# Performance work log

Measured on AMD Instinct MI355X. Metric: run time of the kernel, lower is better.

## Reference

```python
import jax, jax.numpy as jnp
import numpy as np

N = 50000
E = 800000
D = 256
EPS_FA = 0.1      # FAConv eps (x_0 skip weight)
EPS_LN = 1e-5     # LayerNorm eps


def setup_inputs() -> dict:
    key = jax.random.key(0)
    ks = jax.random.split(key, 8)
    node = jax.random.normal(ks[0], (N, D), dtype=jnp.float32)
    node_0 = jax.random.normal(ks[1], (N, D), dtype=jnp.float32)
    edge_index = jax.random.randint(ks[2], (2, E), 0, N, dtype=jnp.int64)
    edge_attr = jax.random.uniform(ks[3], (E,), dtype=jnp.float32)
    batch_ptr = jnp.sort(jax.random.randint(ks[4], (9,), 0, N, dtype=jnp.int64))
    # FAConv attention vectors: Linear(channels, 1, bias=False) -> [D]
    att_l = jax.random.normal(ks[5], (D,), dtype=jnp.float32) / np.sqrt(D)
    att_r = jax.random.normal(ks[6], (D,), dtype=jnp.float32) / np.sqrt(D)
    ln_weight = jnp.ones((D,), dtype=jnp.float32)
    ln_bias = jnp.zeros((D,), dtype=jnp.float32)
    return {"node": node, "node_0": node_0, "edge_index": edge_index,
            "edge_attr": edge_attr, "batch_ptr": batch_ptr,
            "att_l": att_l, "att_r": att_r,
            "ln_weight": ln_weight, "ln_bias": ln_bias}


def reference(node, node_0, edge_index, edge_attr, batch_ptr, att_l, att_r, ln_weight, ln_bias):
    src = edge_index[0]  # j (source)
    dst = edge_index[1]  # i (target)
    # per-node attention scalars
    a_l = node @ att_l   # [N]
    a_r = node @ att_r   # [N]
    # per-edge coefficient: tanh(alpha_j + alpha_i) * edge_weight
    coef = jnp.tanh(a_l[src] + a_r[dst]) * edge_attr          # [E]
    msg = node[src] * coef[:, None]                           # [E, D]
    agg = jax.ops.segment_sum(msg, dst, num_segments=N)       # [N, D]
    out = agg + EPS_FA * node_0
    # LayerNorm (mode='node'): per-node over features; batch_ptr unused in node mode
    mean = out.mean(axis=-1, keepdims=True)
    var = out.var(axis=-1, keepdims=True)
    out = (out - mean) * jax.lax.rsqrt(var + EPS_LN) * ln_weight + ln_bias
    return jax.nn.relu(out)
```

## Files before the change

### kernel.cpp

```cpp
#include <hip/hip_runtime.h>
#include <math.h>

#define NN 50000
#define NE 800000
#define D 256
#define EPS_FA 0.1f
#define EPS_LN 1e-5f
#define MAXDEG 48
#define ALPHA_BLOCKS (NN / 4)
#define EDGE_BLOCKS ((NE + 255) / 256)
#define EB8 ((NE + 2047) / 2048)

typedef unsigned int u32x2 __attribute__((ext_vector_type(2)));
typedef float        f32x4 __attribute__((ext_vector_type(4)));


__device__ __forceinline__ unsigned bf16_bits(float f) {
    unsigned u = __float_as_uint(f);
    u += 0x7FFFu + ((u >> 16) & 1u);
    return u >> 16;
}
__device__ __forceinline__ float bf16_lo(unsigned u) { return __uint_as_float(u << 16); }
__device__ __forceinline__ float bf16_hi(unsigned u) { return __uint_as_float(u & 0xFFFF0000u); }

__device__ __forceinline__ float fast_tanh(float x) {
    x = fminf(fmaxf(x, -15.0f), 15.0f);
    float e2 = __expf(2.0f * x);
    return 1.0f - 2.0f * __fdividef(1.0f, e2 + 1.0f);
}

template<int DS>
__global__ __launch_bounds__(256) void alpha_fill_t(
    const float* __restrict__ node,
    const float* __restrict__ att_l,
    const float* __restrict__ att_r,
    const int*   __restrict__ edge_index,
    const float* __restrict__ edge_attr,
    float* __restrict__ a_l,
    float* __restrict__ a_r,
    uint2* __restrict__ node_bf,
    int*      __restrict__ deg,
    unsigned* __restrict__ slots)
{
    int b = blockIdx.x;
    if (b < EB8) {
        int base = b * 2048 + threadIdx.x;
        int src[8], dst[8];
        unsigned attr[8];
        #pragma unroll
        for (int i = 0; i < 8; i++) {
            int e = base + i * 256;
            bool ok = e < NE;
            src[i]  = ok ? __builtin_nontemporal_load(&edge_index[e]) : 0;
            dst[i]  = ok ? __builtin_nontemporal_load(&edge_index[NE + e]) : -1;
            attr[i] = ok ? bf16_bits(__builtin_nontemporal_load(&edge_attr[e])) : 0u;
        }
        int rank[8];
        #pragma unroll
        for (int i = 0; i < 8; i++)
            rank[i] = (dst[i] >= 0) ? atomicAdd(&deg[dst[i] * DS], 1) : MAXDEG;
        #pragma unroll
        for (int i = 0; i < 8; i++)
            if (dst[i] >= 0 && rank[i] < MAXDEG)
                slots[dst[i] * MAXDEG + rank[i]] = (unsigned)src[i] | (attr[i] << 16);
    } else {
        int wid  = ((b - EB8) * 256 + threadIdx.x) >> 6;
        int lane = threadIdx.x & 63;
        f32x4 v = __builtin_nontemporal_load((const f32x4*)(node + (size_t)wid * D) + lane);
        float4 l = ((const float4*)att_l)[lane];
        float4 r = ((const float4*)att_r)[lane];
        uint2 p;
        p.x = bf16_bits(v.x) | (bf16_bits(v.y) << 16);
        p.y = bf16_bits(v.z) | (bf16_bits(v.w) << 16);
        node_bf[(size_t)wid * 64 + lane] = p;
        float sl = v.x * l.x + v.y * l.y + v.z * l.z + v.w * l.w;
        float sr = v.x * r.x + v.y * r.y + v.z * r.z + v.w * r.w;
        #pragma unroll
        for (int off = 32; off > 0; off >>= 1) {
            sl += __shfl_down(sl, off, 64);
            sr += __shfl_down(sr, off, 64);
        }
        if (lane == 0) { a_l[wid] = sl; a_r[wid] = sr; }
    }
}

template<int DS>
__global__ __launch_bounds__(256) void gather_ln_bf16_t(
    const uint2* __restrict__ node_bf,
    const float* __restrict__ node_0,
    const float* __restrict__ a_l,
    const float* __restrict__ a_r,
    const int*      __restrict__ deg,
    const unsigned* __restrict__ slots,
    const float* __restrict__ w,
    const float* __restrict__ b,
    float* __restrict__ out)
{
    int n    = (blockIdx.x * 256 + threadIdx.x) >> 6;
    int lane = threadIdx.x & 63;

    f32x4 z = __builtin_nontemporal_load((const f32x4*)(node_0 + (size_t)n * D) + lane);
    float4 acc;
    acc.x = EPS_FA * z.x; acc.y = EPS_FA * z.y;
    acc.z = EPS_FA * z.z; acc.w = EPS_FA * z.w;

    int d = min(__builtin_nontemporal_load(&deg[n * DS]), MAXDEG);
    const unsigned* sl = slots + n * MAXDEG;

    unsigned myslot = (lane < d) ? __builtin_nontemporal_load(&sl[lane]) : 0u;
    int      myrow  = (int)(myslot & 0xFFFF);
    float    ar     = a_r[n];
    float    mycoef = 0.0f;
    if (lane < d)
        mycoef = fast_tanh(a_l[myrow] + ar) * bf16_hi(myslot);

    int k = 0;
    for (; k + 15 < d; k += 16) {
        int row[16]; float c[16]; uint2 r[16];
        #pragma unroll
        for (int i = 0; i < 16; i++) {
            row[i] = __shfl(myrow,  k + i, 64);
            c[i]   = __shfl(mycoef, k + i, 64);
        }
        #pragma unroll
        for (int i = 0; i < 16; i++)
            r[i] = node_bf[(size_t)row[i] * 64 + lane];
        #pragma unroll
        for (int i = 0; i < 16; i++) {
            acc.x += c[i] * bf16_lo(r[i].x); acc.y += c[i] * bf16_hi(r[i].x);
            acc.z += c[i] * bf16_lo(r[i].y); acc.w += c[i] * bf16_hi(r[i].y);
        }
    }
    for (; k + 7 < d; k += 8) {
        int row[8]; float c[8]; uint2 r[8];
        #pragma unroll
        for (int i = 0; i < 8; i++) {
            row[i] = __shfl(myrow,  k + i, 64);
            c[i]   = __shfl(mycoef, k + i, 64);
        }
        #pragma unroll
        for (int i = 0; i < 8; i++)
            r[i] = node_bf[(size_t)row[i] * 64 + lane];
        #pragma unroll
        for (int i = 0; i < 8; i++) {
            acc.x += c[i] * bf16_lo(r[i].x); acc.y += c[i] * bf16_hi(r[i].x);
            acc.z += c[i] * bf16_lo(r[i].y); acc.w += c[i] * bf16_hi(r[i].y);
        }
    }
    for (; k + 3 < d; k += 4) {
        int row[4]; float c[4]; uint2 r[4];
        #pragma unroll
        for (int i = 0; i < 4; i++) {
            row[i] = __shfl(myrow,  k + i, 64);
            c[i]   = __shfl(mycoef, k + i, 64);
        }
        #pragma unroll
        for (int i = 0; i < 4; i++)
            r[i] = node_bf[(size_t)row[i] * 64 + lane];
        #pragma unroll
        for (int i = 0; i < 4; i++) {
            acc.x += c[i] * bf16_lo(r[i].x); acc.y += c[i] * bf16_hi(r[i].x);
            acc.z += c[i] * bf16_lo(r[i].y); acc.w += c[i] * bf16_hi(r[i].y);
        }
    }
    for (; k < d; k++) {
        int   row0 = __shfl(myrow,  k, 64);
        float c0   = __shfl(mycoef, k, 64);
        uint2 r0 = node_bf[(size_t)row0 * 64 + lane];
        acc.x += c0 * bf16_lo(r0.x); acc.y += c0 * bf16_hi(r0.x);
        acc.z += c0 * bf16_lo(r0.y); acc.w += c0 * bf16_hi(r0.y);
    }

    float s  = acc.x + acc.y + acc.z + acc.w;
    float s2 = acc.x * acc.x + acc.y * acc.y + acc.z * acc.z + acc.w * acc.w;
    #pragma unroll
    for (int ofs = 1; ofs < 64; ofs <<= 1) {
        s  += __shfl_xor(s,  ofs, 64);
        s2 += __shfl_xor(s2, ofs, 64);
    }
    float mean = s * (1.0f / D);
    float var  = s2 * (1.0f / D) - mean * mean;
    float inv  = rsqrtf(var + EPS_LN);

    float4 wv = ((const float4*)w)[lane];
    float4 bv = ((const float4*)b)[lane];
    float4 o;
    o.x = fmaxf(0.0f, (acc.x - mean) * inv * wv.x + bv.x);
    o.y = fmaxf(0.0f, (acc.y - mean) * inv * wv.y + bv.y);
    o.z = fmaxf(0.0f, (acc.z - mean) * inv * wv.z + bv.z);
    o.w = fmaxf(0.0f, (acc.w - mean) * inv * wv.w + bv.w);
    ((float4*)(out + (size_t)n * D))[lane] = o;
}


__global__ __launch_bounds__(256) void alpha_kernel(
    const float* __restrict__ node,
    const float* __restrict__ att_l,
    const float* __restrict__ att_r,
    float* __restrict__ a_l,
    float* __restrict__ a_r)
{
    int wid  = (blockIdx.x * 256 + threadIdx.x) >> 6;
    int lane = threadIdx.x & 63;
    float4 v = ((const float4*)(node + (size_t)wid * D))[lane];
    float4 l = ((const float4*)att_l)[lane];
    float4 r = ((const float4*)att_r)[lane];
    float sl = v.x * l.x + v.y * l.y + v.z * l.z + v.w * l.w;
    float sr = v.x * r.x + v.y * r.y + v.z * r.z + v.w * r.w;
    #pragma unroll
    for (int off = 32; off > 0; off >>= 1) {
        sl += __shfl_down(sl, off, 64);
        sr += __shfl_down(sr, off, 64);
    }
    if (lane == 0) { a_l[wid] = sl; a_r[wid] = sr; }
}

__global__ __launch_bounds__(256) void hist_kernel(
    const int* __restrict__ edge_index, int* __restrict__ deg)
{
    int e = blockIdx.x * blockDim.x + threadIdx.x;
    if (e < NE) atomicAdd(&deg[edge_index[NE + e]], 1);
}

__global__ __launch_bounds__(256) void start_kernel(
    const int* __restrict__ deg, int* __restrict__ start,
    int* __restrict__ cur, int* __restrict__ total)
{
    int n    = blockIdx.x * blockDim.x + threadIdx.x;
    int lane = threadIdx.x & 63;
    int d = (n < NN) ? deg[n] : 0;
    int pre = d;
    #pragma unroll
    for (int ofs = 1; ofs < 64; ofs <<= 1) {
        int v = __shfl_up(pre, ofs, 64);
        if (lane >= ofs) pre += v;
    }
    int wavesum = __shfl(pre, 63, 64);
    int base = 0;
    if (lane == 63) base = atomicAdd(total, wavesum);
    base = __shfl(base, 63, 64);
    if (n < NN) { int s = base + pre - d; start[n] = s; cur[n] = s; }
}

__global__ __launch_bounds__(256) void fill_csr_kernel(
    const int*   __restrict__ edge_index,
    const float* __restrict__ edge_attr,
    int*      __restrict__ cur,
    unsigned* __restrict__ slots)
{
    int e = blockIdx.x * blockDim.x + threadIdx.x;
    if (e >= NE) return;
    int src = edge_index[e];
    int dst = edge_index[NE + e];
    unsigned attr = bf16_bits(edge_attr[e]);
    int slot = atomicAdd(&cur[dst], 1);
    slots[slot] = (unsigned)src | (attr << 16);
}

__global__ __launch_bounds__(256) void gather_ln_csr_kernel(
    const float* __restrict__ node,
    const float* __restrict__ node_0,
    const float* __restrict__ a_l,
    const float* __restrict__ a_r,
    const int*      __restrict__ start,
    const int*      __restrict__ cur,
    const unsigned* __restrict__ slots,
    const float* __restrict__ w,
    const float* __restrict__ b,
    float* __restrict__ out)
{
    int n    = (blockIdx.x * 256 + threadIdx.x) >> 6;
    int lane = threadIdx.x & 63;

    float4 z = ((const float4*)(node_0 + (size_t)n * D))[lane];
    float4 acc;
    acc.x = EPS_FA * z.x; acc.y = EPS_FA * z.y;
    acc.z = EPS_FA * z.z; acc.w = EPS_FA * z.w;

    int base = start[n];
    int d    = cur[n] - base;
    const unsigned* sl = slots + base;
    float ar = a_r[n];

    for (int k = 0; k < d; k++) {
        unsigned s0 = sl[k];
        int i0 = s0 & 0xFFFF;
        float4 v0 = ((const float4*)node)[(size_t)i0 * 64 + lane];
        float c0 = fast_tanh(a_l[i0] + ar) * bf16_hi(s0);
        acc.x += c0 * v0.x; acc.y += c0 * v0.y; acc.z += c0 * v0.z; acc.w += c0 * v0.w;
    }

    float s  = acc.x + acc.y + acc.z + acc.w;
    float s2 = acc.x * acc.x + acc.y * acc.y + acc.z * acc.z + acc.w * acc.w;
    #pragma unroll
    for (int ofs = 1; ofs < 64; ofs <<= 1) {
        s  += __shfl_xor(s,  ofs, 64);
        s2 += __shfl_xor(s2, ofs, 64);
    }
    float mean = s * (1.0f / D);
    float var  = s2 * (1.0f / D) - mean * mean;
    float inv  = rsqrtf(var + EPS_LN);

    float4 wv = ((const float4*)w)[lane];
    float4 bv = ((const float4*)b)[lane];
    float4 o;
    o.x = fmaxf(0.0f, (acc.x - mean) * inv * wv.x + bv.x);
    o.y = fmaxf(0.0f, (acc.y - mean) * inv * wv.y + bv.y);
    o.z = fmaxf(0.0f, (acc.z - mean) * inv * wv.z + bv.z);
    o.w = fmaxf(0.0f, (acc.w - mean) * inv * wv.w + bv.w);
    ((float4*)(out + (size_t)n * D))[lane] = o;
}

extern "C" void kernel_launch(void* const* d_in, const int* in_sizes, int n_in,
                              void* d_out, int out_size, void* d_ws, size_t ws_size,
                              hipStream_t stream)
{
    const float* node      = (const float*)d_in[0];
    const float* node_0    = (const float*)d_in[1];
    const int*   edge_idx  = (const int*)d_in[2];
    const float* edge_attr = (const float*)d_in[3];
    const float* att_l     = (const float*)d_in[5];
    const float* att_r     = (const float*)d_in[6];
    const float* ln_w      = (const float*)d_in[7];
    const float* ln_b      = (const float*)d_in[8];
    float* out = (float*)d_out;

    const size_t slots_pad_b = (size_t)NN * MAXDEG * 4;
    const size_t bf_b        = (size_t)NN * 64 * 8;
    const size_t smallA_b    = (size_t)NN * (2 + 16) * 4 + 4096;
    const size_t smallB_b    = (size_t)NN * 3 * 4 + 4096;
    const size_t need_A = slots_pad_b + bf_b + smallA_b;
    const size_t need_B = slots_pad_b + bf_b + smallB_b;

    if (ws_size >= need_A) {
        unsigned* slots   = (unsigned*)d_ws;
        uint2*    node_bf = (uint2*)((char*)d_ws + slots_pad_b);
        float*    a_l     = (float*)((char*)node_bf + bf_b);
        float*    a_r     = a_l + NN;
        int*      deg     = (int*)(a_r + NN);

        hipMemsetAsync(deg, 0, (size_t)NN * 16 * sizeof(int), stream);
        alpha_fill_t<16><<<EB8 + ALPHA_BLOCKS, 256, 0, stream>>>(
            node, att_l, att_r, edge_idx, edge_attr, a_l, a_r, node_bf, deg, slots);
        gather_ln_bf16_t<16><<<NN / 4, 256, 0, stream>>>(
            node_bf, node_0, a_l, a_r, deg, slots, ln_w, ln_b, out);
    } else if (ws_size >= need_B) {
        unsigned* slots   = (unsigned*)d_ws;
        uint2*    node_bf = (uint2*)((char*)d_ws + slots_pad_b);
        float*    a_l     = (float*)((char*)node_bf + bf_b);
        float*    a_r     = a_l + NN;
        int*      deg     = (int*)(a_r + NN);

        hipMemsetAsync(deg, 0, NN * sizeof(int), stream);
        alpha_fill_t<1><<<EB8 + ALPHA_BLOCKS, 256, 0, stream>>>(
            node, att_l, att_r, edge_idx, edge_attr, a_l, a_r, node_bf, deg, slots);
        gather_ln_bf16_t<1><<<NN / 4, 256, 0, stream>>>(
            node_bf, node_0, a_l, a_r, deg, slots, ln_w, ln_b, out);
    } else {
        unsigned* slots = (unsigned*)d_ws;
        float*    a_l   = (float*)(slots + NE);
        float*    a_r   = a_l + NN;
        int*      deg   = (int*)(a_r + NN);
        int*      total = deg + NN;
        int*      start = total + 1;
        int*      cur   = start + NN;

        hipMemsetAsync(deg, 0, (NN + 1) * sizeof(int), stream);
        alpha_kernel<<<ALPHA_BLOCKS, 256, 0, stream>>>(
            node, att_l, att_r, a_l, a_r);
        hist_kernel<<<EDGE_BLOCKS, 256, 0, stream>>>(edge_idx, deg);
        start_kernel<<<(NN + 255) / 256, 256, 0, stream>>>(deg, start, cur, total);
        fill_csr_kernel<<<EDGE_BLOCKS, 256, 0, stream>>>(edge_idx, edge_attr, cur, slots);
        gather_ln_csr_kernel<<<NN / 4, 256, 0, stream>>>(
            node, node_0, a_l, a_r, start, cur, slots, ln_w, ln_b, out);
    }
}
```

Before: 250.0 us.

## Pack degree counter and edge slots into one 256-byte per-node record

Puts each node's degree counter in word 0 of a 64-word row and its up-to-48 packed (src, bf16 weight) slots in words 1..48. The gather kernel then reads the count and every slot with one coalesced 64-lane load, instead of a separate degree load followed by a dependent slot load. This gives each node's atomic counter its own 256-byte row, but the memset grows to cover the whole combined buffer and the gather drops its 16-way unrolled loop. The fallback kernels lose their template stride parameter and their nontemporal loads.

```diff
diff --git a/kernel.cpp b/kernel.cpp
--- a/kernel.cpp
+++ b/kernel.cpp
@@ -29,8 +29,7 @@
     return 1.0f - 2.0f * __fdividef(1.0f, e2 + 1.0f);
 }
 
-template<int DS>
-__global__ __launch_bounds__(256) void alpha_fill_t(
+__global__ __launch_bounds__(256) void alpha_fill_comb(
     const float* __restrict__ node,
     const float* __restrict__ att_l,
     const float* __restrict__ att_r,
@@ -39,8 +38,7 @@
     float* __restrict__ a_l,
     float* __restrict__ a_r,
     uint2* __restrict__ node_bf,
-    int*      __restrict__ deg,
-    unsigned* __restrict__ slots)
+    unsigned* __restrict__ comb)
 {
     int b = blockIdx.x;
     if (b < EB8) {
@@ -55,14 +53,14 @@
             dst[i]  = ok ? __builtin_nontemporal_load(&edge_index[NE + e]) : -1;
             attr[i] = ok ? bf16_bits(__builtin_nontemporal_load(&edge_attr[e])) : 0u;
         }
-        int rank[8];
+        unsigned rank[8];
         #pragma unroll
         for (int i = 0; i < 8; i++)
-            rank[i] = (dst[i] >= 0) ? atomicAdd(&deg[dst[i] * DS], 1) : MAXDEG;
+            rank[i] = (dst[i] >= 0) ? atomicAdd(&comb[(size_t)dst[i] * 64], 1u) : MAXDEG;
         #pragma unroll
         for (int i = 0; i < 8; i++)
             if (dst[i] >= 0 && rank[i] < MAXDEG)
-                slots[dst[i] * MAXDEG + rank[i]] = (unsigned)src[i] | (attr[i] << 16);
+                comb[(size_t)dst[i] * 64 + 1 + rank[i]] = (unsigned)src[i] | (attr[i] << 16);
     } else {
         int wid  = ((b - EB8) * 256 + threadIdx.x) >> 6;
         int lane = threadIdx.x & 63;
@@ -84,7 +82,150 @@
     }
 }
 
-template<int DS>
+__global__ __launch_bounds__(256) void gather_ln_comb(
+    const uint2* __restrict__ node_bf,
+    const float* __restrict__ node_0,
+    const float* __restrict__ a_l,
+    const float* __restrict__ a_r,
+    const unsigned* __restrict__ comb,
+    const float* __restrict__ w,
+    const float* __restrict__ b,
+    float* __restrict__ out)
+{
+    int n    = (blockIdx.x * 256 + threadIdx.x) >> 6;
+    int lane = threadIdx.x & 63;
+
+    f32x4 z = __builtin_nontemporal_load((const f32x4*)(node_0 + (size_t)n * D) + lane);
+    float4 acc;
+    acc.x = EPS_FA * z.x; acc.y = EPS_FA * z.y;
+    acc.z = EPS_FA * z.z; acc.w = EPS_FA * z.w;
+
+    unsigned myword = __builtin_nontemporal_load(&comb[(size_t)n * 64 + lane]);
+    int d = min(__shfl((int)myword, 0, 64), MAXDEG);
+
+    bool  own    = (lane >= 1) && (lane <= d);
+    int   myrow  = own ? (int)(myword & 0xFFFFu) : 0;
+    float ar     = a_r[n];
+    float mycoef = 0.0f;
+    if (own) mycoef = fast_tanh(a_l[myrow] + ar) * bf16_hi(myword);
+
+    int k = 0;
+    for (; k + 7 < d; k += 8) {
+        int row[8]; float c[8]; uint2 r[8];
+        #pragma unroll
+        for (int i = 0; i < 8; i++) {
+            row[i] = __shfl(myrow,  k + i + 1, 64);
+            c[i]   = __shfl(mycoef, k + i + 1, 64);
+        }
+        #pragma unroll
+        for (int i = 0; i < 8; i++)
+            r[i] = node_bf[(size_t)row[i] * 64 + lane];
+        #pragma unroll
+        for (int i = 0; i < 8; i++) {
+            acc.x += c[i] * bf16_lo(r[i].x); acc.y += c[i] * bf16_hi(r[i].x);
+            acc.z += c[i] * bf16_lo(r[i].y); acc.w += c[i] * bf16_hi(r[i].y);
+        }
+    }
+    for (; k + 3 < d; k += 4) {
+        int row[4]; float c[4]; uint2 r[4];
+        #pragma unroll
+        for (int i = 0; i < 4; i++) {
+            row[i] = __shfl(myrow,  k + i + 1, 64);
+            c[i]   = __shfl(mycoef, k + i + 1, 64);
+        }
+        #pragma unroll
+        for (int i = 0; i < 4; i++)
+            r[i] = node_bf[(size_t)row[i] * 64 + lane];
+        #pragma unroll
+        for (int i = 0; i < 4; i++) {
+            acc.x += c[i] * bf16_lo(r[i].x); acc.y += c[i] * bf16_hi(r[i].x);
+            acc.z += c[i] * bf16_lo(r[i].y); acc.w += c[i] * bf16_hi(r[i].y);
+        }
+    }
+    for (; k < d; k++) {
+        int   row0 = __shfl(myrow,  k + 1, 64);
+        float c0   = __shfl(mycoef, k + 1, 64);
+        uint2 r0 = node_bf[(size_t)row0 * 64 + lane];
+        acc.x += c0 * bf16_lo(r0.x); acc.y += c0 * bf16_hi(r0.x);
+        acc.z += c0 * bf16_lo(r0.y); acc.w += c0 * bf16_hi(r0.y);
+    }
+
+    float s  = acc.x + acc.y + acc.z + acc.w;
+    float s2 = acc.x * acc.x + acc.y * acc.y + acc.z * acc.z + acc.w * acc.w;
+    #pragma unroll
+    for (int ofs = 1; ofs < 64; ofs <<= 1) {
+        s  += __shfl_xor(s,  ofs, 64);
+        s2 += __shfl_xor(s2, ofs, 64);
+    }
+    float mean = s * (1.0f / D);
+    float var  = s2 * (1.0f / D) - mean * mean;
+    float inv  = rsqrtf(var + EPS_LN);
+
+    float4 wv = ((const float4*)w)[lane];
+    float4 bv = ((const float4*)b)[lane];
+    float4 o;
+    o.x = fmaxf(0.0f, (acc.x - mean) * inv * wv.x + bv.x);
+    o.y = fmaxf(0.0f, (acc.y - mean) * inv * wv.y + bv.y);
+    o.z = fmaxf(0.0f, (acc.z - mean) * inv * wv.z + bv.z);
+    o.w = fmaxf(0.0f, (acc.w - mean) * inv * wv.w + bv.w);
+    ((float4*)(out + (size_t)n * D))[lane] = o;
+}
+
+
+__global__ __launch_bounds__(256) void alpha_fill_t(
+    const float* __restrict__ node,
+    const float* __restrict__ att_l,
+    const float* __restrict__ att_r,
+    const int*   __restrict__ edge_index,
+    const float* __restrict__ edge_attr,
+    float* __restrict__ a_l,
+    float* __restrict__ a_r,
+    uint2* __restrict__ node_bf,
+    int*      __restrict__ deg,
+    unsigned* __restrict__ slots)
+{
+    int b = blockIdx.x;
+    if (b < EB8) {
+        int base = b * 2048 + threadIdx.x;
+        int src[8], dst[8];
+        unsigned attr[8];
+        #pragma unroll
+        for (int i = 0; i < 8; i++) {
+            int e = base + i * 256;
+            bool ok = e < NE;
+            src[i]  = ok ? edge_index[e] : 0;
+            dst[i]  = ok ? edge_index[NE + e] : -1;
+            attr[i] = ok ? bf16_bits(edge_attr[e]) : 0u;
+        }
+        int rank[8];
+        #pragma unroll
+        for (int i = 0; i < 8; i++)
+            rank[i] = (dst[i] >= 0) ? atomicAdd(&deg[dst[i]], 1) : MAXDEG;
+        #pragma unroll
+        for (int i = 0; i < 8; i++)
+            if (dst[i] >= 0 && rank[i] < MAXDEG)
+                slots[dst[i] * MAXDEG + rank[i]] = (unsigned)src[i] | (attr[i] << 16);
+    } else {
+        int wid  = ((b - EB8) * 256 + threadIdx.x) >> 6;
+        int lane = threadIdx.x & 63;
+        float4 v = ((const float4*)(node + (size_t)wid * D))[lane];
+        float4 l = ((const float4*)att_l)[lane];
+        float4 r = ((const float4*)att_r)[lane];
+        uint2 p;
+        p.x = bf16_bits(v.x) | (bf16_bits(v.y) << 16);
+        p.y = bf16_bits(v.z) | (bf16_bits(v.w) << 16);
+        node_bf[(size_t)wid * 64 + lane] = p;
+        float sl = v.x * l.x + v.y * l.y + v.z * l.z + v.w * l.w;
+        float sr = v.x * r.x + v.y * r.y + v.z * r.z + v.w * r.w;
+        #pragma unroll
+        for (int off = 32; off > 0; off >>= 1) {
+            sl += __shfl_down(sl, off, 64);
+            sr += __shfl_down(sr, off, 64);
+        }
+        if (lane == 0) { a_l[wid] = sl; a_r[wid] = sr; }
+    }
+}
+
 __global__ __launch_bounds__(256) void gather_ln_bf16_t(
     const uint2* __restrict__ node_bf,
     const float* __restrict__ node_0,
@@ -99,15 +240,15 @@
     int n    = (blockIdx.x * 256 + threadIdx.x) >> 6;
     int lane = threadIdx.x & 63;
 
-    f32x4 z = __builtin_nontemporal_load((const f32x4*)(node_0 + (size_t)n * D) + lane);
+    float4 z = ((const float4*)(node_0 + (size_t)n * D))[lane];
     float4 acc;
     acc.x = EPS_FA * z.x; acc.y = EPS_FA * z.y;
     acc.z = EPS_FA * z.z; acc.w = EPS_FA * z.w;
 
-    int d = min(__builtin_nontemporal_load(&deg[n * DS]), MAXDEG);
+    int d = min(deg[n], MAXDEG);
     const unsigned* sl = slots + n * MAXDEG;
 
-    unsigned myslot = (lane < d) ? __builtin_nontemporal_load(&sl[lane]) : 0u;
+    unsigned myslot = (lane < d) ? sl[lane] : 0u;
     int      myrow  = (int)(myslot & 0xFFFF);
     float    ar     = a_r[n];
     float    mycoef = 0.0f;
@@ -115,22 +256,6 @@
         mycoef = fast_tanh(a_l[myrow] + ar) * bf16_hi(myslot);
 
     int k = 0;
-    for (; k + 15 < d; k += 16) {
-        int row[16]; float c[16]; uint2 r[16];
-        #pragma unroll
-        for (int i = 0; i < 16; i++) {
-            row[i] = __shfl(myrow,  k + i, 64);
-            c[i]   = __shfl(mycoef, k + i, 64);
-        }
-        #pragma unroll
-        for (int i = 0; i < 16; i++)
-            r[i] = node_bf[(size_t)row[i] * 64 + lane];
-        #pragma unroll
-        for (int i = 0; i < 16; i++) {
-            acc.x += c[i] * bf16_lo(r[i].x); acc.y += c[i] * bf16_hi(r[i].x);
-            acc.z += c[i] * bf16_lo(r[i].y); acc.w += c[i] * bf16_hi(r[i].y);
-        }
-    }
     for (; k + 7 < d; k += 8) {
         int row[8]; float c[8]; uint2 r[8];
         #pragma unroll
@@ -325,25 +450,23 @@
     const float* ln_b      = (const float*)d_in[8];
     float* out = (float*)d_out;
 
+    const size_t comb_b      = (size_t)NN * 64 * 4;
+    const size_t bf_b        = (size_t)NN * 64 * 8;
     const size_t slots_pad_b = (size_t)NN * MAXDEG * 4;
-    const size_t bf_b        = (size_t)NN * 64 * 8;
-    const size_t smallA_b    = (size_t)NN * (2 + 16) * 4 + 4096;
-    const size_t smallB_b    = (size_t)NN * 3 * 4 + 4096;
-    const size_t need_A = slots_pad_b + bf_b + smallA_b;
-    const size_t need_B = slots_pad_b + bf_b + smallB_b;
+    const size_t need_A = comb_b + bf_b + (size_t)NN * 2 * 4 + 4096;
+    const size_t need_B = slots_pad_b + bf_b + (size_t)NN * 3 * 4 + 4096;
 
     if (ws_size >= need_A) {
-        unsigned* slots   = (unsigned*)d_ws;
-        uint2*    node_bf = (uint2*)((char*)d_ws + slots_pad_b);
+        unsigned* comb    = (unsigned*)d_ws;
+        uint2*    node_bf = (uint2*)((char*)d_ws + comb_b);
         float*    a_l     = (float*)((char*)node_bf + bf_b);
         float*    a_r     = a_l + NN;
-        int*      deg     = (int*)(a_r + NN);
-
-        hipMemsetAsync(deg, 0, (size_t)NN * 16 * sizeof(int), stream);
-        alpha_fill_t<16><<<EB8 + ALPHA_BLOCKS, 256, 0, stream>>>(
-            node, att_l, att_r, edge_idx, edge_attr, a_l, a_r, node_bf, deg, slots);
-        gather_ln_bf16_t<16><<<NN / 4, 256, 0, stream>>>(
-            node_bf, node_0, a_l, a_r, deg, slots, ln_w, ln_b, out);
+
+        hipMemsetAsync(comb, 0, comb_b, stream);
+        alpha_fill_comb<<<EB8 + ALPHA_BLOCKS, 256, 0, stream>>>(
+            node, att_l, att_r, edge_idx, edge_attr, a_l, a_r, node_bf, comb);
+        gather_ln_comb<<<NN / 4, 256, 0, stream>>>(
+            node_bf, node_0, a_l, a_r, comb, ln_w, ln_b, out);
     } else if (ws_size >= need_B) {
         unsigned* slots   = (unsigned*)d_ws;
         uint2*    node_bf = (uint2*)((char*)d_ws + slots_pad_b);
@@ -352,9 +475,9 @@
         int*      deg     = (int*)(a_r + NN);
 
         hipMemsetAsync(deg, 0, NN * sizeof(int), stream);
-        alpha_fill_t<1><<<EB8 + ALPHA_BLOCKS, 256, 0, stream>>>(
+        alpha_fill_t<<<EB8 + ALPHA_BLOCKS, 256, 0, stream>>>(
             node, att_l, att_r, edge_idx, edge_attr, a_l, a_r, node_bf, deg, slots);
-        gather_ln_bf16_t<1><<<NN / 4, 256, 0, stream>>>(
+        gather_ln_bf16_t<<<NN / 4, 256, 0, stream>>>(
             node_bf, node_0, a_l, a_r, deg, slots, ln_w, ln_b, out);
     } else {
         unsigned* slots = (unsigned*)d_ws;
```

New measurement: 252.3 us. No clear change (+0.9%).
